# Kernel optimization log

Measured on AMD Instinct MI355X. Metric: run time of the kernel, lower is better.

## Reference

```python
import jax, jax.numpy as jnp
import numpy as np

B, S, E, H = 2, 2048, 512, 8
D = E // H  # head size = 64
LN_EPS = 1e-5


def setup_inputs() -> dict:
    key = jax.random.key(0)
    ks = jax.random.split(key, 8)
    s_in = 1.0 / np.sqrt(E)
    return {
        "x": jax.random.normal(ks[0], (B, S, E), jnp.float32),
        # per-head projection weights, stored [H, E, D] so q = x @ Wq[h]
        "Wq": jax.random.normal(ks[1], (H, E, D), jnp.float32) * s_in,
        "Wk": jax.random.normal(ks[2], (H, E, D), jnp.float32) * s_in,
        "Wv": jax.random.normal(ks[3], (H, E, D), jnp.float32) * s_in,
        "Wp": jax.random.normal(ks[4], (E, E), jnp.float32) * s_in,
        "bp": jnp.zeros((E,), jnp.float32),
        "gamma": jnp.ones((E,), jnp.float32),
        "beta": jnp.zeros((E,), jnp.float32),
        # causal mask buffer: masked_fill where mask == 0
        "mask": jnp.tril(jnp.ones((S, S), jnp.int32)),
    }


def reference(x, Wq, Wk, Wv, Wp, bp, gamma, beta, mask):
    # batched per-head projections (equivalent to the H small Linears)
    q = jnp.einsum("bse,hed->bhsd", x, Wq)
    k = jnp.einsum("bse,hed->bhsd", x, Wk)
    v = jnp.einsum("bse,hed->bhsd", x, Wv)
    # NOTE: original has NO 1/sqrt(d) scaling
    att_log = jnp.einsum("bhsd,bhtd->bhst", q, k)
    att_log = jnp.where(mask == 0, -jnp.inf, att_log)
    att = jax.nn.softmax(att_log, axis=-1)
    o = jnp.einsum("bhst,bhtd->bhsd", att, v)  # [B,H,S,D]
    # torch.cat((val, values)) prepends each head -> final order head H-1 .. 0
    o = o[:, ::-1]
    vals = o.transpose(0, 2, 1, 3).reshape(B, S, E)
    out = vals @ Wp.T + bp + x
    mu = jnp.mean(out, axis=-1, keepdims=True)
    var = jnp.var(out, axis=-1, keepdims=True)
    return (out - mu) * jax.lax.rsqrt(var + LN_EPS) * gamma + beta
```

## Files before the change

### kernel.cpp

```cpp
#include <hip/hip_runtime.h>

constexpr int Bn = 2;
constexpr int Sn = 2048;
constexpr int En = 512;
constexpr int Hn = 8;
constexpr int Dn = 64;
constexpr int Mn = Bn * Sn;

typedef short bf8 __attribute__((ext_vector_type(8)));
typedef float f32x4 __attribute__((ext_vector_type(4)));

constexpr size_t XY = (size_t)Mn * En;
constexpr size_t WT = (size_t)3 * En * En;
constexpr size_t WP = (size_t)En * En;
constexpr size_t PL = (size_t)Bn * Hn * Sn * Dn;

__device__ __forceinline__ unsigned short f2bf(float f) {
    unsigned int u = __float_as_uint(f);
    unsigned int r = 0x7FFFu + ((u >> 16) & 1u);
    return (unsigned short)((u + r) >> 16);
}
__device__ __forceinline__ float bf2f(unsigned short u) {
    return __uint_as_float(((unsigned int)u) << 16);
}
__device__ __forceinline__ void split2(float f, unsigned short& hi, unsigned short& lo) {
    hi = f2bf(f);
    lo = f2bf(f - bf2f(hi));
}

__device__ __forceinline__ void g2l16(const unsigned short* g, unsigned short* l) {
    typedef __attribute__((address_space(1))) const unsigned int gu32;
    typedef __attribute__((address_space(3))) unsigned int lu32;
    __builtin_amdgcn_global_load_lds((gu32*)(unsigned long long)g,
                                     (lu32*)(unsigned int)(unsigned long long)l,
                                     16, 0, 0);
}

__global__ __launch_bounds__(256)
void prep(const float* __restrict__ x, const float* __restrict__ Wp,
          const float* __restrict__ Wq, const float* __restrict__ Wk,
          const float* __restrict__ Wv,
          unsigned short* __restrict__ xh, unsigned short* __restrict__ xl,
          unsigned short* __restrict__ Wph, unsigned short* __restrict__ Wpl,
          unsigned short* __restrict__ Wth, unsigned short* __restrict__ Wtl)
{
    __shared__ float t[64][65];
    const int bid = blockIdx.x;
    const int tid = threadIdx.x;

    if (bid < 1152) {
        const float* src = (bid < 1024) ? x : Wp;
        unsigned short* hp = (bid < 1024) ? xh : Wph;
        unsigned short* lp = (bid < 1024) ? xl : Wpl;
        const int blk = (bid < 1024) ? bid : (bid - 1024);
        const size_t base = ((size_t)blk * 256 + tid) * 8;
        float a[8];
        *(float4*)&a[0] = *(const float4*)(src + base);
        *(float4*)&a[4] = *(const float4*)(src + base + 4);
        unsigned short h[8], l[8];
        #pragma unroll
        for (int j = 0; j < 8; ++j) split2(a[j], h[j], l[j]);
        *(bf8*)(hp + base) = *(bf8*)&h[0];
        *(bf8*)(lp + base) = *(bf8*)&l[0];
        return;
    }

    const int idx = bid - 1152;
    const int ph = idx >> 3;
    const int proj = ph >> 3, h = ph & 7;
    const int e0 = (idx & 7) * 64;
    const float* W = (proj == 0) ? Wq : (proj == 1) ? Wk : Wv;
    const float* src = W + (size_t)h * En * Dn + (size_t)e0 * Dn;

    const int er = tid >> 2, cg = (tid & 3) * 16;
    #pragma unroll
    for (int c = 0; c < 4; ++c) {
        float4 v = *(const float4*)(src + (size_t)er * Dn + cg + 4 * c);
        t[er][cg + 4 * c + 0] = v.x;
        t[er][cg + 4 * c + 1] = v.y;
        t[er][cg + 4 * c + 2] = v.z;
        t[er][cg + 4 * c + 3] = v.w;
    }
    __syncthreads();

    const int d = tid >> 2, jg = (tid & 3) * 16;
    unsigned short h16[16], l16[16];
    #pragma unroll
    for (int j = 0; j < 16; ++j) split2(t[jg + j][d], h16[j], l16[j]);
    const size_t n = (size_t)proj * 512 + h * 64 + d;
    unsigned short* dh = Wth + n * En + e0 + jg;
    unsigned short* dl = Wtl + n * En + e0 + jg;
    *(bf8*)dh       = *(bf8*)&h16[0];
    *(bf8*)(dh + 8) = *(bf8*)&h16[8];
    *(bf8*)dl       = *(bf8*)&l16[0];
    *(bf8*)(dl + 8) = *(bf8*)&l16[8];
}

__global__ __launch_bounds__(256)
void qkv_gemm(const unsigned short* __restrict__ xh,
              const unsigned short* __restrict__ xl,
              const unsigned short* __restrict__ Wth,
              const unsigned short* __restrict__ Wtl,
              unsigned short* __restrict__ qh_g,
              unsigned short* __restrict__ ql_g,
              unsigned short* __restrict__ kh_g,
              unsigned short* __restrict__ kl_g,
              unsigned short* __restrict__ vT_g)
{
    __shared__ __align__(16) unsigned char smraw[49152];
    unsigned short* ldsAh = (unsigned short*)smraw;
    unsigned short* ldsAl = ldsAh + 8192;
    unsigned short* ldsBh = ldsAl + 8192;
    unsigned short* ldsBl = ldsBh + 4096;
    float (*Cf)[68] = (float(*)[68])(smraw);

    const int tid = threadIdx.x;
    const int m0 = blockIdx.x * 128;
    const int ny = blockIdx.y;
    const int proj = ny >> 3, h = ny & 7;

    const int wave = tid >> 6, lane = tid & 63;
    const int wm = (wave >> 1) * 64, wn = (wave & 1) * 32;
    const int lm = lane & 15, quad = lane >> 4;

    const int l4r = lane >> 2;
    const int l4c = (lane & 3) * 8;
    const unsigned short* gAh0 = xh + (size_t)(m0 + wave * 32 + l4r) * En + l4c;
    const unsigned short* gAh1 = gAh0 + (size_t)16 * En;
    const unsigned short* gAl0 = xl + (size_t)(m0 + wave * 32 + l4r) * En + l4c;
    const unsigned short* gAl1 = gAl0 + (size_t)16 * En;
    const unsigned short* gBh  = Wth + (size_t)(ny * 64 + wave * 16 + l4r) * En + l4c;
    const unsigned short* gBl  = Wtl + (size_t)(ny * 64 + wave * 16 + l4r) * En + l4c;
    const int offA = wave * 1024;
    const int offB = wave * 512;

    f32x4 acc[4][2];
    #pragma unroll
    for (int i = 0; i < 4; ++i)
        #pragma unroll
        for (int j = 0; j < 2; ++j) acc[i][j] = (f32x4){0.f, 0.f, 0.f, 0.f};

    g2l16(gAh0, ldsAh + offA);
    g2l16(gAh1, ldsAh + offA + 512);
    g2l16(gAl0, ldsAl + offA);
    g2l16(gAl1, ldsAl + offA + 512);
    g2l16(gBh,  ldsBh + offB);
    g2l16(gBl,  ldsBl + offB);

    int cur = 0;
    for (int k0 = 0; k0 < En; k0 += 32) {
        __syncthreads();
        const int nxt = cur ^ 1;
        if (k0 + 32 < En) {
            g2l16(gAh0 + k0 + 32, ldsAh + nxt * 4096 + offA);
            g2l16(gAh1 + k0 + 32, ldsAh + nxt * 4096 + offA + 512);
            g2l16(gAl0 + k0 + 32, ldsAl + nxt * 4096 + offA);
            g2l16(gAl1 + k0 + 32, ldsAl + nxt * 4096 + offA + 512);
            g2l16(gBh + k0 + 32,  ldsBh + nxt * 2048 + offB);
            g2l16(gBl + k0 + 32,  ldsBl + nxt * 2048 + offB);
        }

        const unsigned short* bAh = ldsAh + cur * 4096;
        const unsigned short* bAl = ldsAl + cur * 4096;
        const unsigned short* bBh = ldsBh + cur * 2048;
        const unsigned short* bBl = ldsBl + cur * 2048;
        bf8 a_h[4], a_l[4], b_h[2], b_l[2];
        #pragma unroll
        for (int mi = 0; mi < 4; ++mi) {
            a_h[mi] = *(const bf8*)(bAh + (wm + mi * 16 + lm) * 32 + quad * 8);
            a_l[mi] = *(const bf8*)(bAl + (wm + mi * 16 + lm) * 32 + quad * 8);
        }
        #pragma unroll
        for (int ni = 0; ni < 2; ++ni) {
            b_h[ni] = *(const bf8*)(bBh + (wn + ni * 16 + lm) * 32 + quad * 8);
            b_l[ni] = *(const bf8*)(bBl + (wn + ni * 16 + lm) * 32 + quad * 8);
        }
        #pragma unroll
        for (int mi = 0; mi < 4; ++mi)
            #pragma unroll
            for (int ni = 0; ni < 2; ++ni) {
                acc[mi][ni] = __builtin_amdgcn_mfma_f32_16x16x32_bf16(a_h[mi], b_h[ni], acc[mi][ni], 0, 0, 0);
                acc[mi][ni] = __builtin_amdgcn_mfma_f32_16x16x32_bf16(a_h[mi], b_l[ni], acc[mi][ni], 0, 0, 0);
                acc[mi][ni] = __builtin_amdgcn_mfma_f32_16x16x32_bf16(a_l[mi], b_h[ni], acc[mi][ni], 0, 0, 0);
            }
        cur = nxt;
    }
    __syncthreads();

    if (proj < 2) {
        unsigned short* hp = (proj == 0) ? qh_g : kh_g;
        unsigned short* lp = (proj == 0) ? ql_g : kl_g;
        #pragma unroll
        for (int p = 0; p < 2; ++p) {
            if ((wave >> 1) == p) {
                #pragma unroll
                for (int mi = 0; mi < 4; ++mi)
                    #pragma unroll
                    for (int ni = 0; ni < 2; ++ni)
                        #pragma unroll
                        for (int r = 0; r < 4; ++r)
                            Cf[mi * 16 + quad * 4 + r][wn + ni * 16 + lm] = acc[mi][ni][r];
            }
            __syncthreads();
            {
                const int lr = tid & 63;
                const int cg = (tid >> 6) * 16;
                const int m = m0 + p * 64 + lr;
                const int b = m >> 11, s = m & 2047;
                unsigned short hi[16], lo[16];
                #pragma unroll
                for (int j4 = 0; j4 < 4; ++j4) {
                    float4 v = *(const float4*)&Cf[lr][cg + 4 * j4];
                    split2(v.x, hi[4 * j4 + 0], lo[4 * j4 + 0]);
                    split2(v.y, hi[4 * j4 + 1], lo[4 * j4 + 1]);
                    split2(v.z, hi[4 * j4 + 2], lo[4 * j4 + 2]);
                    split2(v.w, hi[4 * j4 + 3], lo[4 * j4 + 3]);
                }
                const size_t base = (((size_t)(b * Hn + h) * Sn + s) * Dn) + cg;
                *(bf8*)(hp + base)     = *(bf8*)&hi[0];
                *(bf8*)(hp + base + 8) = *(bf8*)&hi[8];
                *(bf8*)(lp + base)     = *(bf8*)&lo[0];
                *(bf8*)(lp + base + 8) = *(bf8*)&lo[8];
            }
            __syncthreads();
        }
    } else {
        #pragma unroll
        for (int mi = 0; mi < 4; ++mi) {
            const int s0 = m0 + wm + mi * 16 + quad * 4;
            const int b = s0 >> 11, s = s0 & 2047;
            #pragma unroll
            for (int ni = 0; ni < 2; ++ni) {
                const int d = wn + ni * 16 + lm;
                ushort4 pk;
                pk.x = f2bf(acc[mi][ni][0]);
                pk.y = f2bf(acc[mi][ni][1]);
                pk.z = f2bf(acc[mi][ni][2]);
                pk.w = f2bf(acc[mi][ni][3]);
                *(ushort4*)(vT_g + ((size_t)(b * Hn + h) * Dn + d) * Sn + s) = pk;
            }
        }
    }
}

__global__ __launch_bounds__(512, 4)
void attn(const unsigned short* __restrict__ qh_g,
          const unsigned short* __restrict__ ql_g,
          const unsigned short* __restrict__ kh_g,
          const unsigned short* __restrict__ kl_g,
          const unsigned short* __restrict__ vT_g,
          unsigned short* __restrict__ Op,
          float* __restrict__ ml)
{
    extern __shared__ unsigned short sm[];
    unsigned short (*khs)[72] = (unsigned short(*)[72])(sm);
    unsigned short (*kls)[72] = (unsigned short(*)[72])(sm + 4608);
    unsigned short (*vTs)[72] = (unsigned short(*)[72])(sm + 9216);
    unsigned short (*pts)[72] = (unsigned short(*)[72])(sm + 13824);
    float* alf = (float*)(sm + 23040);

    const int bidx = blockIdx.x;
    const int xcd = bidx & 7;
    const int g = bidx >> 3;
    const int bh = xcd * 2 + (g & 1);
    const int qp = g >> 1;

    const int tid = threadIdx.x;
    const int wave = tid >> 6, lane = tid & 63;
    const int quad = lane >> 4, lq = lane & 15;
    const int wq = wave >> 2;
    const int w4 = wave & 3;

    const unsigned short* khb = kh_g + (size_t)bh * Sn * Dn;
    const unsigned short* klb = kl_g + (size_t)bh * Sn * Dn;
    const unsigned short* vTb = vT_g + (size_t)bh * Dn * Sn;

    const int srow = tid & 63;
    const int sdg  = tid >> 6;

    #pragma unroll 1
    for (int ph = 0; ph < 2; ++ph) {
        const int qt  = ph ? (15 - qp) : qp;
        const int its = ph ? (qt + 1) : 0;
        const int ite = ph ? (2 * qt + 2) : (qt + 1);
        const int qt64 = 2 * qt + wq;
        const int pslot = ph * 512 + bh * 32 + qt64;
        const int dt = qt64;

        bf8 qfh[2], qfl[2];
        {
            const size_t qoff = ((size_t)bh * Sn + (size_t)qt * 128 + wave * 16 + lq) * Dn;
            #pragma unroll
            for (int c = 0; c < 2; ++c) {
                qfh[c] = *(const bf8*)(qh_g + qoff + c * 32 + quad * 8);
                qfl[c] = *(const bf8*)(ql_g + qoff + c * 32 + quad * 8);
            }
        }

        f32x4 accO[4];
        #pragma unroll
        for (int nj = 0; nj < 4; ++nj) accO[nj] = (f32x4){0.f, 0.f, 0.f, 0.f};
        float m = -1e30f, l = 0.f;

        bf8 pk0, pl0, pv0;
        {
            const int t0 = its * 64;
            pk0 = *(const bf8*)(khb + (size_t)(t0 + srow) * Dn + sdg * 8);
            pl0 = *(const bf8*)(klb + (size_t)(t0 + srow) * Dn + sdg * 8);
            pv0 = *(const bf8*)(vTb + (size_t)srow * Sn + t0 + sdg * 8);
        }

        for (int it = its; it < ite; ++it) {
            __syncthreads();
            *(bf8*)&khs[srow][sdg * 8] = pk0;
            *(bf8*)&kls[srow][sdg * 8] = pl0;
            *(bf8*)&vTs[srow][sdg * 8] = pv0;
            __syncthreads();

            if (it + 1 < ite) {
                const int t1 = (it + 1) * 64;
                pk0 = *(const bf8*)(khb + (size_t)(t1 + srow) * Dn + sdg * 8);
                pl0 = *(const bf8*)(klb + (size_t)(t1 + srow) * Dn + sdg * 8);
                pv0 = *(const bf8*)(vTb + (size_t)srow * Sn + t1 + sdg * 8);
            }

            if (it > dt) continue;

            f32x4 accS[4];
            #pragma unroll
            for (int mi = 0; mi < 4; ++mi) accS[mi] = (f32x4){0.f, 0.f, 0.f, 0.f};
            __builtin_amdgcn_s_setprio(1);
            #pragma unroll
            for (int mi = 0; mi < 4; ++mi) {
                #pragma unroll
                for (int c = 0; c < 2; ++c) {
                    bf8 ah = *(const bf8*)&khs[mi * 16 + lq][c * 32 + quad * 8];
                    bf8 al = *(const bf8*)&kls[mi * 16 + lq][c * 32 + quad * 8];
                    accS[mi] = __builtin_amdgcn_mfma_f32_16x16x32_bf16(ah, qfh[c], accS[mi], 0, 0, 0);
                    accS[mi] = __builtin_amdgcn_mfma_f32_16x16x32_bf16(ah, qfl[c], accS[mi], 0, 0, 0);
                    accS[mi] = __builtin_amdgcn_mfma_f32_16x16x32_bf16(al, qfh[c], accS[mi], 0, 0, 0);
                }
            }
            __builtin_amdgcn_s_setprio(0);

            if (it == dt) {
                const int qrel = w4 * 16 + lq;
                #pragma unroll
                for (int mi = 0; mi < 4; ++mi)
                    #pragma unroll
                    for (int r = 0; r < 4; ++r)
                        if (mi * 16 + quad * 4 + r > qrel) accS[mi][r] = -INFINITY;
            }

            float mt;
            {
                float t0 = fmaxf(fmaxf(accS[0][0], accS[0][1]), fmaxf(accS[0][2], accS[0][3]));
                float t1 = fmaxf(fmaxf(accS[1][0], accS[1][1]), fmaxf(accS[1][2], accS[1][3]));
                float t2 = fmaxf(fmaxf(accS[2][0], accS[2][1]), fmaxf(accS[2][2], accS[2][3]));
                float t3 = fmaxf(fmaxf(accS[3][0], accS[3][1]), fmaxf(accS[3][2], accS[3][3]));
                mt = fmaxf(fmaxf(t0, t1), fmaxf(t2, t3));
            }
            mt = fmaxf(mt, __shfl_xor(mt, 16));
            mt = fmaxf(mt, __shfl_xor(mt, 32));

            const bool defer = __all(mt <= m + 12.f);
            float mref, alpha = 1.f;
            if (defer) {
                mref = m;
            } else {
                mref = fmaxf(m, mt);
                alpha = __expf(m - mref);
            }

            float ls = 0.f;
            #pragma unroll
            for (int mi = 0; mi < 4; ++mi)
                #pragma unroll
                for (int r = 0; r < 4; ++r) {
                    const float p = __expf(accS[mi][r] - mref);
                    accS[mi][r] = p;
                    ls += p;
                }
            ls += __shfl_xor(ls, 16);
            ls += __shfl_xor(ls, 32);
            if (defer) {
                l += ls;
            } else {
                l = l * alpha + ls;
                m = mref;
            }

            #pragma unroll
            for (int mi = 0; mi < 4; ++mi) {
                ushort4 pk;
                pk.x = f2bf(accS[mi][0]);
                pk.y = f2bf(accS[mi][1]);
                pk.z = f2bf(accS[mi][2]);
                pk.w = f2bf(accS[mi][3]);
                *(ushort4*)&pts[wave * 16 + lq][mi * 16 + quad * 4] = pk;
            }

            if (!defer) {
                if (quad == 0) alf[wave * 16 + lq] = alpha;
                float4 al4 = *(const float4*)&alf[wave * 16 + quad * 4];
                #pragma unroll
                for (int nj = 0; nj < 4; ++nj) {
                    accO[nj][0] *= al4.x;
                    accO[nj][1] *= al4.y;
                    accO[nj][2] *= al4.z;
                    accO[nj][3] *= al4.w;
                }
            }

            __builtin_amdgcn_s_setprio(1);
            #pragma unroll
            for (int c = 0; c < 2; ++c) {
                bf8 pf = *(const bf8*)&pts[wave * 16 + lq][c * 32 + quad * 8];
                #pragma unroll
                for (int nj = 0; nj < 4; ++nj) {
                    bf8 vf = *(const bf8*)&vTs[nj * 16 + lq][c * 32 + quad * 8];
                    accO[nj] = __builtin_amdgcn_mfma_f32_16x16x32_bf16(pf, vf, accO[nj], 0, 0, 0);
                }
            }
            __builtin_amdgcn_s_setprio(0);
        }

        if (quad == 0) {
            const size_t mi_ = ((size_t)pslot * 64 + w4 * 16 + lq) * 2;
            ml[mi_]     = m;
            ml[mi_ + 1] = l;
        }
        #pragma unroll
        for (int r = 0; r < 4; ++r) {
            const int q = w4 * 16 + quad * 4 + r;
            unsigned short* dst = Op + ((size_t)pslot * 64 + q) * 64;
            #pragma unroll
            for (int nj = 0; nj < 4; ++nj)
                dst[nj * 16 + lq] = f2bf(accO[nj][r]);
        }
    }
}

__global__ __launch_bounds__(256)
void out_gemm(const unsigned short* __restrict__ Op,
              const float* __restrict__ ml,
              const unsigned short* __restrict__ Wph,
              const unsigned short* __restrict__ Wpl,
              const float* __restrict__ bp,
              const float* __restrict__ x,
              float* __restrict__ outp,
              float* __restrict__ outp2)
{
    __shared__ unsigned short Ah[64][40], Al[64][40];
    __shared__ __align__(16) unsigned short Bh[128][32], Bl[128][32];

    const int tid = threadIdx.x;
    const int m0 = blockIdx.x * 64;
    const int n0 = blockIdx.y * 128;
    const int kz = blockIdx.z;
    const int kbeg = kz * 256, kend = kbeg + 256;

    const int wave = tid >> 6, lane = tid & 63;
    const int wm = (wave >> 1) * 32, wn = (wave & 1) * 64;
    const int lm = lane & 15, quad = lane >> 4;

    const int am = tid >> 2;
    const int aks = (tid & 3) * 8;
    const int m_row = m0 + am;
    const int b_row = m_row >> 11, s_row = m_row & 2047;
    const int qt = s_row >> 6, qq = s_row & 63;

    float c0[8], c1[8];
    #pragma unroll
    for (int h = 0; h < 8; ++h) {
        const size_t base0 = (((size_t)(b_row * 8 + h) * 32 + qt) * 64 + qq) * 2;
        const size_t base1 = base0 + (size_t)512 * 64 * 2;
        const float m0_ = ml[base0], l0_ = ml[base0 + 1];
        const float m1_ = ml[base1], l1_ = ml[base1 + 1];
        const float mn = fmaxf(m0_, m1_);
        const float a0 = __expf(m0_ - mn), a1 = __expf(m1_ - mn);
        const float inv = 1.f / (a0 * l0_ + a1 * l1_);
        c0[h] = a0 * inv;
        c1[h] = a1 * inv;
    }

    const int l4r = lane >> 2;
    const int l4c = (lane & 3) * 8;
    const unsigned short* gB0h = Wph + (size_t)(n0 + wave * 32 + l4r) * En + l4c;
    const unsigned short* gB1h = gB0h + (size_t)16 * En;
    const unsigned short* gB0l = Wpl + (size_t)(n0 + wave * 32 + l4r) * En + l4c;
    const unsigned short* gB1l = gB0l + (size_t)16 * En;
    unsigned short* dB0h = &Bh[0][0] + wave * 1024;
    unsigned short* dB1h = dB0h + 512;
    unsigned short* dB0l = &Bl[0][0] + wave * 1024;
    unsigned short* dB1l = dB0l + 512;

    f32x4 acc[2][4];
    #pragma unroll
    for (int i = 0; i < 2; ++i)
        #pragma unroll
        for (int j = 0; j < 4; ++j) acc[i][j] = (f32x4){0.f, 0.f, 0.f, 0.f};

    bf8 po0, po1;
    {
        const int e0 = kbeg + aks;
        const int hh = 7 - (e0 >> 6);
        const int dd = e0 & 63;
        const size_t p0 = (((size_t)((b_row * 8 + hh) * 32 + qt)) * 64 + qq) * 64 + dd;
        po0 = *(const bf8*)(Op + p0);
        po1 = *(const bf8*)(Op + p0 + (size_t)512 * 64 * 64);
    }

    for (int k0 = kbeg; k0 < kend; k0 += 32) {
        g2l16(gB0h + k0, dB0h);
        g2l16(gB1h + k0, dB1h);
        g2l16(gB0l + k0, dB0l);
        g2l16(gB1l + k0, dB1l);
        {
            const int h_cur = 7 - ((k0 + aks) >> 6);
            const float w0 = c0[h_cur], w1 = c1[h_cur];
            unsigned short hi[8], lo[8];
            #pragma unroll
            for (int j = 0; j < 8; ++j) {
                const float v = w0 * bf2f((unsigned short)po0[j]) +
                                w1 * bf2f((unsigned short)po1[j]);
                split2(v, hi[j], lo[j]);
            }
            *(bf8*)&Ah[am][aks] = *(bf8*)&hi[0];
            *(bf8*)&Al[am][aks] = *(bf8*)&lo[0];
        }
        __syncthreads();

        if (k0 + 32 < kend) {
            const int e0 = k0 + 32 + aks;
            const int hh = 7 - (e0 >> 6);
            const int dd = e0 & 63;
            const size_t p0 = (((size_t)((b_row * 8 + hh) * 32 + qt)) * 64 + qq) * 64 + dd;
            po0 = *(const bf8*)(Op + p0);
            po1 = *(const bf8*)(Op + p0 + (size_t)512 * 64 * 64);
        }

        bf8 a_h[2], a_l[2], b_h[4], b_l[4];
        #pragma unroll
        for (int mi = 0; mi < 2; ++mi) {
            a_h[mi] = *(const bf8*)&Ah[wm + mi * 16 + lm][quad * 8];
            a_l[mi] = *(const bf8*)&Al[wm + mi * 16 + lm][quad * 8];
        }
        #pragma unroll
        for (int ni = 0; ni < 4; ++ni) {
            b_h[ni] = *(const bf8*)&Bh[wn + ni * 16 + lm][quad * 8];
            b_l[ni] = *(const bf8*)&Bl[wn + ni * 16 + lm][quad * 8];
        }
        #pragma unroll
        for (int mi = 0; mi < 2; ++mi)
            #pragma unroll
            for (int ni = 0; ni < 4; ++ni) {
                acc[mi][ni] = __builtin_amdgcn_mfma_f32_16x16x32_bf16(a_h[mi], b_h[ni], acc[mi][ni], 0, 0, 0);
                acc[mi][ni] = __builtin_amdgcn_mfma_f32_16x16x32_bf16(a_h[mi], b_l[ni], acc[mi][ni], 0, 0, 0);
                acc[mi][ni] = __builtin_amdgcn_mfma_f32_16x16x32_bf16(a_l[mi], b_h[ni], acc[mi][ni], 0, 0, 0);
            }
        __syncthreads();
    }

    float* dst = kz ? outp2 : outp;
    #pragma unroll
    for (int mi = 0; mi < 2; ++mi) {
        #pragma unroll
        for (int r = 0; r < 4; ++r) {
            const int m = m0 + wm + mi * 16 + quad * 4 + r;
            #pragma unroll
            for (int ni = 0; ni < 4; ++ni) {
                const int n = n0 + wn + ni * 16 + lm;
                const size_t idx = (size_t)m * En + n;
                const float extra = kz ? 0.f : (bp[n] + x[idx]);
                dst[idx] = acc[mi][ni][r] + extra;
            }
        }
    }
}

__global__ __launch_bounds__(256)
void ln_kernel(const float* __restrict__ outp,
               const float* __restrict__ outp2,
               const float* __restrict__ gamma,
               const float* __restrict__ beta,
               float* __restrict__ y)
{
    const int row = blockIdx.x * 4 + (threadIdx.x >> 6);
    const int lane = threadIdx.x & 63;
    const size_t off = (size_t)row * En + lane * 8;

    float a[8], b2[8];
    *(float4*)&a[0] = *(const float4*)(outp + off);
    *(float4*)&a[4] = *(const float4*)(outp + off + 4);
    *(float4*)&b2[0] = *(const float4*)(outp2 + off);
    *(float4*)&b2[4] = *(const float4*)(outp2 + off + 4);
    #pragma unroll
    for (int j = 0; j < 8; ++j) a[j] += b2[j];

    float sum = 0.f, sq = 0.f;
    #pragma unroll
    for (int j = 0; j < 8; ++j) { sum += a[j]; sq += a[j] * a[j]; }
    #pragma unroll
    for (int off_ = 1; off_ < 64; off_ <<= 1) {
        sum += __shfl_xor(sum, off_);
        sq  += __shfl_xor(sq, off_);
    }
    const float mu = sum * (1.f / 512.f);
    const float var = sq * (1.f / 512.f) - mu * mu;
    const float rs = rsqrtf(var + 1e-5f);

    const float* g = gamma + lane * 8;
    const float* be = beta + lane * 8;
    float o[8];
    #pragma unroll
    for (int j = 0; j < 8; ++j)
        o[j] = (a[j] - mu) * rs * g[j] + be[j];
    float* yr = y + off;
    *(float4*)(yr)     = *(float4*)&o[0];
    *(float4*)(yr + 4) = *(float4*)&o[4];
}

extern "C" void kernel_launch(void* const* d_in, const int* in_sizes, int n_in,
                              void* d_out, int out_size, void* d_ws, size_t ws_size,
                              hipStream_t stream)
{
    const float* x     = (const float*)d_in[0];
    const float* Wq    = (const float*)d_in[1];
    const float* Wk    = (const float*)d_in[2];
    const float* Wv    = (const float*)d_in[3];
    const float* Wp    = (const float*)d_in[4];
    const float* bp    = (const float*)d_in[5];
    const float* gamma = (const float*)d_in[6];
    const float* beta  = (const float*)d_in[7];

    float* ws   = (float*)d_ws;
    float* ml   = ws;
    float* outp = ws + XY;
    unsigned short* bfb = (unsigned short*)(ws + 2 * XY);
    unsigned short* xh  = bfb;
    unsigned short* xl  = bfb + XY;
    unsigned short* Wth = bfb + 2 * XY;
    unsigned short* Wtl = Wth + WT;
    unsigned short* Wph = Wtl + WT;
    unsigned short* Wpl = Wph + WP;
    unsigned short* qh  = Wpl + WP;
    unsigned short* ql  = qh + PL;
    unsigned short* kh  = ql + PL;
    unsigned short* kl  = kh + PL;
    unsigned short* vT  = kl + PL;
    unsigned short* Op = xh;
    float* outp2 = (float*)qh;

    const int attn_lds = 46592;
    hipFuncSetAttribute((const void*)attn,
                        hipFuncAttributeMaxDynamicSharedMemorySize, attn_lds);

    prep<<<dim3(1344), 256, 0, stream>>>(x, Wp, Wq, Wk, Wv,
                                         xh, xl, Wph, Wpl, Wth, Wtl);
    qkv_gemm<<<dim3(Mn / 128, 24), 256, 0, stream>>>(xh, xl, Wth, Wtl,
                                                     qh, ql, kh, kl, vT);
    attn<<<dim3(256), 512, attn_lds, stream>>>(qh, ql, kh, kl, vT, Op, ml);
    out_gemm<<<dim3(Mn / 64, En / 128, 2), 256, 0, stream>>>(Op, ml, Wph, Wpl,
                                                             bp, x, outp, outp2);
    ln_kernel<<<dim3(Mn / 4), 256, 0, stream>>>(outp, outp2, gamma, beta,
                                                (float*)d_out);
}
```

Baseline: 172.2 us.

## Split attention KV range into four partials and merge them in output GEMM

The attention kernel now splits each query tile's key range into four chunks instead of two, and launches twice as many blocks. Each block writes partial outputs and (m,l) statistics per chunk. The output GEMM combines four partials with rescaling weights instead of two. The partial output buffer moves to a dedicated workspace region so it no longer aliases xh. The aim is better load balance and occupancy on the GPU, at the cost of more partial-output traffic and extra combine arithmetic in the GEMM prologue.

```diff
diff --git a/kernel.cpp b/kernel.cpp
--- a/kernel.cpp
+++ b/kernel.cpp
@@ -14,6 +14,8 @@
 constexpr size_t WT = (size_t)3 * En * En;
 constexpr size_t WP = (size_t)En * En;
 constexpr size_t PL = (size_t)Bn * Hn * Sn * Dn;
+constexpr size_t MLP = (size_t)512 * 64 * 2;
+constexpr size_t OPP = (size_t)512 * 64 * 64;
 
 __device__ __forceinline__ unsigned short f2bf(float f) {
     unsigned int u = __float_as_uint(f);
@@ -263,7 +265,9 @@
     const int xcd = bidx & 7;
     const int g = bidx >> 3;
     const int bh = xcd * 2 + (g & 1);
-    const int qp = g >> 1;
+    const int p2 = g >> 1;
+    const int qp = p2 & 15;
+    const int sb = p2 >> 4;
 
     const int tid = threadIdx.x;
     const int wave = tid >> 6, lane = tid & 63;
@@ -280,11 +284,13 @@
 
     #pragma unroll 1
     for (int ph = 0; ph < 2; ++ph) {
-        const int qt  = ph ? (15 - qp) : qp;
-        const int its = ph ? (qt + 1) : 0;
-        const int ite = ph ? (2 * qt + 2) : (qt + 1);
+        const int qt = ph ? (15 - qp) : qp;
+        const int j  = ph ? (3 - sb) : sb;
+        const int n  = 2 * qt + 2;
+        const int its = (j * n) >> 2;
+        const int ite = ((j + 1) * n) >> 2;
         const int qt64 = 2 * qt + wq;
-        const int pslot = ph * 512 + bh * 32 + qt64;
+        const int pslot = j * 512 + bh * 32 + qt64;
         const int dt = qt64;
 
         bf8 qfh[2], qfl[2];
@@ -302,8 +308,10 @@
         for (int nj = 0; nj < 4; ++nj) accO[nj] = (f32x4){0.f, 0.f, 0.f, 0.f};
         float m = -1e30f, l = 0.f;
 
-        bf8 pk0, pl0, pv0;
-        {
+        bf8 pk0 = {0, 0, 0, 0, 0, 0, 0, 0};
+        bf8 pl0 = {0, 0, 0, 0, 0, 0, 0, 0};
+        bf8 pv0 = {0, 0, 0, 0, 0, 0, 0, 0};
+        if (its < ite) {
             const int t0 = its * 64;
             pk0 = *(const bf8*)(khb + (size_t)(t0 + srow) * Dn + sdg * 8);
             pl0 = *(const bf8*)(klb + (size_t)(t0 + srow) * Dn + sdg * 8);
@@ -470,18 +478,25 @@
     const int b_row = m_row >> 11, s_row = m_row & 2047;
     const int qt = s_row >> 6, qq = s_row & 63;
 
-    float c0[8], c1[8];
-    #pragma unroll
-    for (int h = 0; h < 8; ++h) {
+    float c0[4], c1[4], c2[4], c3[4];
+    #pragma unroll
+    for (int hl = 0; hl < 4; ++hl) {
+        const int h = hl + (kz ? 0 : 4);
         const size_t base0 = (((size_t)(b_row * 8 + h) * 32 + qt) * 64 + qq) * 2;
-        const size_t base1 = base0 + (size_t)512 * 64 * 2;
-        const float m0_ = ml[base0], l0_ = ml[base0 + 1];
-        const float m1_ = ml[base1], l1_ = ml[base1 + 1];
-        const float mn = fmaxf(m0_, m1_);
-        const float a0 = __expf(m0_ - mn), a1 = __expf(m1_ - mn);
-        const float inv = 1.f / (a0 * l0_ + a1 * l1_);
-        c0[h] = a0 * inv;
-        c1[h] = a1 * inv;
+        float mi_[4], li_[4];
+        #pragma unroll
+        for (int i = 0; i < 4; ++i) {
+            mi_[i] = ml[base0 + i * MLP];
+            li_[i] = ml[base0 + i * MLP + 1];
+        }
+        const float mn = fmaxf(fmaxf(mi_[0], mi_[1]), fmaxf(mi_[2], mi_[3]));
+        const float a0 = __expf(mi_[0] - mn), a1 = __expf(mi_[1] - mn);
+        const float a2 = __expf(mi_[2] - mn), a3 = __expf(mi_[3] - mn);
+        const float inv = 1.f / (a0 * li_[0] + a1 * li_[1] + a2 * li_[2] + a3 * li_[3]);
+        c0[hl] = a0 * inv;
+        c1[hl] = a1 * inv;
+        c2[hl] = a2 * inv;
+        c3[hl] = a3 * inv;
     }
 
     const int l4r = lane >> 2;
@@ -501,14 +516,16 @@
         #pragma unroll
         for (int j = 0; j < 4; ++j) acc[i][j] = (f32x4){0.f, 0.f, 0.f, 0.f};
 
-    bf8 po0, po1;
+    bf8 po0, po1, po2, po3;
     {
         const int e0 = kbeg + aks;
         const int hh = 7 - (e0 >> 6);
         const int dd = e0 & 63;
         const size_t p0 = (((size_t)((b_row * 8 + hh) * 32 + qt)) * 64 + qq) * 64 + dd;
         po0 = *(const bf8*)(Op + p0);
-        po1 = *(const bf8*)(Op + p0 + (size_t)512 * 64 * 64);
+        po1 = *(const bf8*)(Op + p0 + OPP);
+        po2 = *(const bf8*)(Op + p0 + 2 * OPP);
+        po3 = *(const bf8*)(Op + p0 + 3 * OPP);
     }
 
     for (int k0 = kbeg; k0 < kend; k0 += 32) {
@@ -517,13 +534,16 @@
         g2l16(gB0l + k0, dB0l);
         g2l16(gB1l + k0, dB1l);
         {
-            const int h_cur = 7 - ((k0 + aks) >> 6);
-            const float w0 = c0[h_cur], w1 = c1[h_cur];
+            const int hidx = (7 - ((k0 + aks) >> 6)) & 3;
+            const float w0 = c0[hidx], w1 = c1[hidx];
+            const float w2 = c2[hidx], w3 = c3[hidx];
             unsigned short hi[8], lo[8];
             #pragma unroll
             for (int j = 0; j < 8; ++j) {
                 const float v = w0 * bf2f((unsigned short)po0[j]) +
-                                w1 * bf2f((unsigned short)po1[j]);
+                                w1 * bf2f((unsigned short)po1[j]) +
+                                w2 * bf2f((unsigned short)po2[j]) +
+                                w3 * bf2f((unsigned short)po3[j]);
                 split2(v, hi[j], lo[j]);
             }
             *(bf8*)&Ah[am][aks] = *(bf8*)&hi[0];
@@ -537,7 +557,9 @@
             const int dd = e0 & 63;
             const size_t p0 = (((size_t)((b_row * 8 + hh) * 32 + qt)) * 64 + qq) * 64 + dd;
             po0 = *(const bf8*)(Op + p0);
-            po1 = *(const bf8*)(Op + p0 + (size_t)512 * 64 * 64);
+            po1 = *(const bf8*)(Op + p0 + OPP);
+            po2 = *(const bf8*)(Op + p0 + 2 * OPP);
+            po3 = *(const bf8*)(Op + p0 + 3 * OPP);
         }
 
         bf8 a_h[2], a_l[2], b_h[4], b_l[4];
@@ -649,7 +671,7 @@
     unsigned short* kh  = ql + PL;
     unsigned short* kl  = kh + PL;
     unsigned short* vT  = kl + PL;
-    unsigned short* Op = xh;
+    unsigned short* Op  = vT + PL;
     float* outp2 = (float*)qh;
 
     const int attn_lds = 46592;
@@ -660,7 +682,7 @@
                                          xh, xl, Wph, Wpl, Wth, Wtl);
     qkv_gemm<<<dim3(Mn / 128, 24), 256, 0, stream>>>(xh, xl, Wth, Wtl,
                                                      qh, ql, kh, kl, vT);
-    attn<<<dim3(256), 512, attn_lds, stream>>>(qh, ql, kh, kl, vT, Op, ml);
+    attn<<<dim3(512), 512, attn_lds, stream>>>(qh, ql, kh, kl, vT, Op, ml);
     out_gemm<<<dim3(Mn / 64, En / 128, 2), 256, 0, stream>>>(Op, ml, Wph, Wpl,
                                                              bp, x, outp, outp2);
     ln_kernel<<<dim3(Mn / 4), 256, 0, stream>>>(outp, outp2, gamma, beta,
```

Result: no change. 170.7 us (median of 2 runs) (-0.9%).
